# Kernel optimization log

Measured on AMD Instinct MI355X. Metric: run time of the kernel, lower is better.

## Reference

```python
import math
import jax, jax.numpy as jnp
import numpy as np

N_HEADS = 8

def setup_inputs() -> dict:
    key = jax.random.key(0)
    bs, n_heads, ch, l = 4, N_HEADS, 64, 1024
    width = 3 * n_heads * ch      # 1536 (packed q,k,v channels)
    T = 3 * l                     # 3072 (three spatial bands: ll, lh, hl)
    qkv = jax.random.normal(key, (bs, width, T), dtype=jnp.float32)
    return {"qkv": qkv, "l": l}

def reference(qkv, l):
    n_heads = N_HEADS
    bs, width, T = qkv.shape
    ch = width // (3 * n_heads)
    q, k, v = jnp.split(qkv, 3, axis=1)              # each (bs, n_heads*ch, T)
    scale = 1.0 / math.sqrt(math.sqrt(ch))
    qh = (q * scale).reshape(bs * n_heads, ch, T)
    kh = (k * scale).reshape(bs * n_heads, ch, T)
    vh = v.reshape(bs * n_heads, ch, T)
    # The original computes attention separately for q[:, :, :l], [l:2l], [2l:],
    # but k/v (and the softmax axis s) are identical, so computing attention
    # over the full query once and splitting the output is the same math.
    attn = jnp.einsum('bct,bcs->bts', qh, kh)        # (bs*H, T, T)
    w = jax.nn.softmax(attn.astype(jnp.float32), axis=-1).astype(attn.dtype)
    agg = jnp.einsum('bts,bcs->bct', w, vh).reshape(bs, n_heads * ch, T)
    return (agg[:, :, :l], agg[:, :, l:2 * l], agg[:, :, 2 * l:])
```

## Files before the change

### kernel.cpp

```cpp
#include <hip/hip_runtime.h>
#include <hip/hip_bf16.h>
#include <stdint.h>

#define T      3072
#define CH     64
#define HEADS  32
#define BM     128
#define BN     64
#define NIT    (T / BN)

typedef unsigned short u16;
typedef short short8 __attribute__((ext_vector_type(8)));
typedef float floatx4 __attribute__((ext_vector_type(4)));

__device__ __forceinline__ unsigned pk2(float a, float b) {
  union { __hip_bfloat162 h; unsigned u; } cv;
  cv.h = __float22bfloat162_rn(float2{a, b});
  return cv.u;
}

__device__ __forceinline__ void gl_lds16(const void* g, void* l) {
  __builtin_amdgcn_global_load_lds(
      (const __attribute__((address_space(1))) uint32_t*)g,
      (__attribute__((address_space(3))) uint32_t*)l, 16, 0, 0);
}

__device__ __forceinline__ void pl32swap(unsigned& x, unsigned& y) {
#if __has_builtin(__builtin_amdgcn_permlane32_swap)
  auto r = __builtin_amdgcn_permlane32_swap(x, y, false, false);
  x = r[0]; y = r[1];
#else
  asm("v_permlane32_swap_b32 %0, %1" : "+v"(x), "+v"(y));
#endif
}
__device__ __forceinline__ void pl16swap(unsigned& x, unsigned& y) {
#if __has_builtin(__builtin_amdgcn_permlane16_swap)
  auto r = __builtin_amdgcn_permlane16_swap(x, y, false, false);
  x = r[0]; y = r[1];
#else
  asm("v_permlane16_swap_b32 %0, %1" : "+v"(x), "+v"(y));
#endif
}

__global__ __launch_bounds__(256) void qktrans(
    const float* __restrict__ qkv, u16* __restrict__ Qt, u16* __restrict__ Kt,
    u16* __restrict__ Vo) {
  __shared__ __align__(16) u16 tl[64][72];
  const int ttile = blockIdx.x, hh = blockIdx.y, role = blockIdx.z;
  const int b = hh >> 3, h = hh & 7;
  const int t0 = ttile * 64;
  const int tid = threadIdx.x;

  if (role == 2) {
    const float* vsrc = qkv + (size_t)(b * 1536 + 1024 + h * CH) * T;
    u16* vdst = Vo + (size_t)(b * 512 + h * CH) * T;
#pragma unroll
    for (int p = 0; p < 2; ++p) {
      const int r = p * 32 + (tid >> 3);
      const int off = (tid & 7) * 8;
      const float4* s4 = (const float4*)(vsrc + (size_t)r * T + t0 + off);
      float4 a = s4[0], c = s4[1];
      uint4 o;
      o.x = pk2(a.x, a.y); o.y = pk2(a.z, a.w);
      o.z = pk2(c.x, c.y); o.w = pk2(c.z, c.w);
      *(uint4*)(vdst + (size_t)r * T + t0 + off) = o;
    }
    return;
  }

  const float* src = qkv + (size_t)(b * 1536 + role * 512 + h * CH) * T;
  const float scale = (role == 0) ? 0.18033688011112042f : 1.0f;

#pragma unroll
  for (int p = 0; p < 2; ++p) {
    const int c0 = p * 32 + ((tid >> 4) << 1);
    const int ts = (tid & 15) * 4;
    float4 a = *(const float4*)(src + (size_t)c0 * T + t0 + ts);
    float4 c = *(const float4*)(src + (size_t)(c0 + 1) * T + t0 + ts);
    *(unsigned*)&tl[ts + 0][c0] = pk2(a.x * scale, c.x * scale);
    *(unsigned*)&tl[ts + 1][c0] = pk2(a.y * scale, c.y * scale);
    *(unsigned*)&tl[ts + 2][c0] = pk2(a.z * scale, c.z * scale);
    *(unsigned*)&tl[ts + 3][c0] = pk2(a.w * scale, c.w * scale);
  }
  __syncthreads();
  u16* dst = (role == 0 ? Qt : Kt) + (size_t)hh * T * CH;
#pragma unroll
  for (int q = 0; q < 2; ++q) {
    const int t = q * 32 + (tid >> 3);
    const int cc = (tid & 7) * 8;
    uint4 v = *(const uint4*)&tl[t][cc];
    *(uint4*)(dst + (size_t)(t0 + t) * CH + cc) = v;
  }
}

__global__ __launch_bounds__(512, 6) void attn(
    const u16* __restrict__ Qt, const u16* __restrict__ Kt,
    const u16* __restrict__ Vg, float* __restrict__ out) {
  __shared__ __align__(16) u16 KB[2][BN * CH];
  __shared__ __align__(16) u16 VB[2][CH * BN];

  const int qtile = blockIdx.x, hh = blockIdx.y;
  const int tid = threadIdx.x;
  const int wave = tid >> 6, lane = tid & 63;
  const int l15 = lane & 15, quad = lane >> 4;
  const int t0 = qtile * BM + wave * 16;

  const u16* Qh = Qt + (size_t)hh * T * CH;
  const u16* Kh = Kt + (size_t)hh * T * CH;
  const u16* Vh = Vg + (size_t)hh * CH * T;

  short8 qf[2];
#pragma unroll
  for (int kc = 0; kc < 2; ++kc)
    qf[kc] = *(const short8*)(Qh + (size_t)(t0 + l15) * CH + kc * 32 + quad * 8);

  short8 ones = {0x3F80, 0x3F80, 0x3F80, 0x3F80, 0x3F80, 0x3F80, 0x3F80, 0x3F80};

  floatx4 oacc[4] = {};
  floatx4 lacc = {0.f, 0.f, 0.f, 0.f};

  const int p = wave * 64 + lane;
  const int srow = p >> 3;
  const int scb = (p & 7) ^ ((srow + 2 * (srow >> 3)) & 7);
  const int swl = (l15 + 2 * (l15 >> 3)) & 7;

#define STAGE(buf, s0)                                                              \
  do {                                                                              \
    gl_lds16(Kh + (size_t)((s0) + srow) * CH + scb * 8,                             \
             &KB[buf][(wave * 64) * 8]);                                            \
    gl_lds16(Vh + (size_t)srow * T + (s0) + scb * 8,                                \
             &VB[buf][(wave * 64) * 8]);                                            \
  } while (0)

  STAGE(0, 0);

  for (int it = 0; it < NIT; ++it) {
    const int cur = it & 1;
    __syncthreads();
    if (it + 1 < NIT) STAGE(cur ^ 1, (it + 1) * BN);

    const u16* KL = KB[cur];
    const u16* VL = VB[cur];

    floatx4 sacc[4];
#pragma unroll
    for (int nt = 0; nt < 4; ++nt) {
      const int ph0 = quad ^ swl ^ ((nt & 1) * 4);
      const int base = (nt * 16 + l15) * CH;
      const short8 kf0 = *(const short8*)(KL + base + ph0 * 8);
      const short8 kf1 = *(const short8*)(KL + base + (ph0 ^ 4) * 8);
      floatx4 z = {0.f, 0.f, 0.f, 0.f};
      z = __builtin_amdgcn_mfma_f32_16x16x32_bf16(kf0, qf[0], z, 0, 0, 0);
      z = __builtin_amdgcn_mfma_f32_16x16x32_bf16(kf1, qf[1], z, 0, 0, 0);
      sacc[nt] = z;
    }

    unsigned Apk[4], Bpk[4];
#pragma unroll
    for (int nt = 0; nt < 4; ++nt) {
      floatx4 sv = sacc[nt];
      float p0 = __builtin_amdgcn_exp2f(sv[0]);
      float p1 = __builtin_amdgcn_exp2f(sv[1]);
      float p2 = __builtin_amdgcn_exp2f(sv[2]);
      float p3 = __builtin_amdgcn_exp2f(sv[3]);
      Apk[nt] = pk2(p0, p1);
      Bpk[nt] = pk2(p2, p3);
    }

#pragma unroll
    for (int ks = 0; ks < 2; ++ks) {
      unsigned a0 = Apk[2 * ks], a1 = Apk[2 * ks + 1];
      unsigned b0 = Bpk[2 * ks], b1 = Bpk[2 * ks + 1];
      pl32swap(a0, a1); pl16swap(a0, a1);
      pl32swap(b0, b1); pl16swap(b0, b1);
      union { uint4 u; short8 s; } pw;
      pw.u.x = a0; pw.u.y = b0; pw.u.z = a1; pw.u.w = b1;
      const short8 pf = pw.s;
      lacc = __builtin_amdgcn_mfma_f32_16x16x32_bf16(pf, ones, lacc, 0, 0, 0);
#pragma unroll
      for (int mt = 0; mt < 4; ++mt) {
        const int ph = quad ^ swl ^ ((mt & 1) * 4) ^ (ks * 4);
        const short8 vf = *(const short8*)(VL + (mt * 16 + l15) * BN + ph * 8);
        oacc[mt] = __builtin_amdgcn_mfma_f32_16x16x32_bf16(pf, vf, oacc[mt], 0, 0, 0);
      }
    }
  }

  float linv[4];
#pragma unroll
  for (int r = 0; r < 4; ++r) linv[r] = 1.0f / lacc[r];

  const int b = hh >> 3, h = hh & 7;
  const int tg = t0 + quad * 4;
  const int band = tg >> 10, tt = tg & 1023;
  float* obase = out + (size_t)band * (4 * 512 * 1024)
                     + (size_t)b * (512 * 1024)
                     + (size_t)(h * CH) * 1024 + tt;
#pragma unroll
  for (int mt = 0; mt < 4; ++mt) {
    const int c = mt * 16 + l15;
    float4 v;
    v.x = oacc[mt][0] * linv[0];
    v.y = oacc[mt][1] * linv[1];
    v.z = oacc[mt][2] * linv[2];
    v.w = oacc[mt][3] * linv[3];
    *(float4*)(obase + (size_t)c * 1024) = v;
  }
}

extern "C" void kernel_launch(void* const* d_in, const int* in_sizes, int n_in,
                              void* d_out, int out_size, void* d_ws, size_t ws_size,
                              hipStream_t stream) {
  (void)in_sizes; (void)n_in; (void)out_size; (void)ws_size;
  const float* qkv = (const float*)d_in[0];
  u16* Qt = (u16*)d_ws;
  u16* Kt = Qt + (size_t)HEADS * T * CH;
  u16* Vo = Kt + (size_t)HEADS * T * CH;
  float* out = (float*)d_out;

  qktrans<<<dim3(T / 64, HEADS, 3), 256, 0, stream>>>(qkv, Qt, Kt, Vo);
  attn<<<dim3(T / BM, HEADS), 512, 0, stream>>>(Qt, Kt, Vo, out);
}
```

Baseline: 214.3 us.

## Load V fragments directly from global memory and remap blocks for XCD locality

Drops the LDS staging buffer for V, so each wave now reads its V MFMA operands straight from global memory (through L2) instead of through a shared double buffer. The grid becomes 1D and is remapped so that all query tiles of a given head land on the same XCD, which is meant to improve L2 reuse of K and V. This halves LDS use and async copy traffic, but every wave now issues redundant uncoalesced global loads of V that sit directly on the MFMA critical path.

```diff
diff --git a/kernel.cpp b/kernel.cpp
--- a/kernel.cpp
+++ b/kernel.cpp
@@ -97,13 +97,17 @@
     const u16* __restrict__ Qt, const u16* __restrict__ Kt,
     const u16* __restrict__ Vg, float* __restrict__ out) {
   __shared__ __align__(16) u16 KB[2][BN * CH];
-  __shared__ __align__(16) u16 VB[2][CH * BN];
-
-  const int qtile = blockIdx.x, hh = blockIdx.y;
+
+  const int lin = blockIdx.x;
+  const int jj = lin >> 3, xcd = lin & 7;
+  const int qtile = jj % 24;
+  const int hh = xcd + 8 * (jj / 24);
+
   const int tid = threadIdx.x;
   const int wave = tid >> 6, lane = tid & 63;
   const int l15 = lane & 15, quad = lane >> 4;
   const int t0 = qtile * BM + wave * 16;
+  const int b = hh >> 3, h = hh & 7;
 
   const u16* Qh = Qt + (size_t)hh * T * CH;
   const u16* Kh = Kt + (size_t)hh * T * CH;
@@ -114,33 +118,29 @@
   for (int kc = 0; kc < 2; ++kc)
     qf[kc] = *(const short8*)(Qh + (size_t)(t0 + l15) * CH + kc * 32 + quad * 8);
 
-  short8 ones = {0x3F80, 0x3F80, 0x3F80, 0x3F80, 0x3F80, 0x3F80, 0x3F80, 0x3F80};
+  const short8 ones = {0x3F80, 0x3F80, 0x3F80, 0x3F80, 0x3F80, 0x3F80, 0x3F80, 0x3F80};
 
   floatx4 oacc[4] = {};
   floatx4 lacc = {0.f, 0.f, 0.f, 0.f};
 
-  const int p = wave * 64 + lane;
-  const int srow = p >> 3;
-  const int scb = (p & 7) ^ ((srow + 2 * (srow >> 3)) & 7);
+  const int srow = tid >> 3;
+  const int scb = (tid & 7) ^ ((srow + 2 * (srow >> 3)) & 7);
   const int swl = (l15 + 2 * (l15 >> 3)) & 7;
-
-#define STAGE(buf, s0)                                                              \
-  do {                                                                              \
-    gl_lds16(Kh + (size_t)((s0) + srow) * CH + scb * 8,                             \
-             &KB[buf][(wave * 64) * 8]);                                            \
-    gl_lds16(Vh + (size_t)srow * T + (s0) + scb * 8,                                \
-             &VB[buf][(wave * 64) * 8]);                                            \
-  } while (0)
-
-  STAGE(0, 0);
+  const int wsl = wave * 512;
+
+#define STAGE_K(kb, s0) \
+  gl_lds16(Kh + (size_t)((s0) + srow) * CH + scb * 8, &KB[kb][wsl])
+
+  const u16* Vp = Vh + (size_t)l15 * T + quad * 8;
+
+  STAGE_K(0, 0);
 
   for (int it = 0; it < NIT; ++it) {
     const int cur = it & 1;
     __syncthreads();
-    if (it + 1 < NIT) STAGE(cur ^ 1, (it + 1) * BN);
+    if (it + 1 < NIT) STAGE_K(cur ^ 1, (it + 1) * BN);
 
     const u16* KL = KB[cur];
-    const u16* VL = VB[cur];
 
     floatx4 sacc[4];
 #pragma unroll
@@ -167,6 +167,7 @@
       Bpk[nt] = pk2(p2, p3);
     }
 
+    const u16* Vit = Vp + it * BN;
 #pragma unroll
     for (int ks = 0; ks < 2; ++ks) {
       unsigned a0 = Apk[2 * ks], a1 = Apk[2 * ks + 1];
@@ -179,8 +180,7 @@
       lacc = __builtin_amdgcn_mfma_f32_16x16x32_bf16(pf, ones, lacc, 0, 0, 0);
 #pragma unroll
       for (int mt = 0; mt < 4; ++mt) {
-        const int ph = quad ^ swl ^ ((mt & 1) * 4) ^ (ks * 4);
-        const short8 vf = *(const short8*)(VL + (mt * 16 + l15) * BN + ph * 8);
+        const short8 vf = *(const short8*)(Vit + (size_t)(mt * 16) * T + ks * 32);
         oacc[mt] = __builtin_amdgcn_mfma_f32_16x16x32_bf16(pf, vf, oacc[mt], 0, 0, 0);
       }
     }
@@ -190,7 +190,6 @@
 #pragma unroll
   for (int r = 0; r < 4; ++r) linv[r] = 1.0f / lacc[r];
 
-  const int b = hh >> 3, h = hh & 7;
   const int tg = t0 + quad * 4;
   const int band = tg >> 10, tt = tg & 1023;
   float* obase = out + (size_t)band * (4 * 512 * 1024)
@@ -219,5 +218,5 @@
   float* out = (float*)d_out;
 
   qktrans<<<dim3(T / 64, HEADS, 3), 256, 0, stream>>>(qkv, Qt, Kt, Vo);
-  attn<<<dim3(T / BM, HEADS), 512, 0, stream>>>(Qt, Kt, Vo, out);
-}
+  attn<<<dim3(768), 512, 0, stream>>>(Qt, Kt, Vo, out);
+}
```

After: 380.8 us. 77.7% more time.
